# Optimization experiments

Hardware: AMD Instinct MI355X
Metric: run time of the kernel (lower is better)

Reference implementation:

```python
import jax, jax.numpy as jnp
import numpy as np


def reference(x, weight, bias):
    """Per-sample dynamic conv2d, expressed as one grouped convolution.

    x:      (B, C_in, H, W)
    weight: (B, C_out, C_in, kH, kW)
    bias:   (B, C_out)
    returns (B, C_out, H_out, W_out) with H_out = H - kH + 1 (valid conv)
    """
    B, C_in, H, W = x.shape
    C_out, kH, kW = weight.shape[1], weight.shape[3], weight.shape[4]
    # Fold batch into channels: groups=B grouped conv == B independent convs.
    x_g = x.reshape(1, B * C_in, H, W)
    w_g = weight.reshape(B * C_out, C_in, kH, kW)
    out = jax.lax.conv_general_dilated(
        x_g, w_g,
        window_strides=(1, 1),
        padding='VALID',
        dimension_numbers=('NCHW', 'OIHW', 'NCHW'),
        feature_group_count=B,
    )  # (1, B*C_out, H_out, W_out)
    out = out.reshape(B, C_out, out.shape[2], out.shape[3])
    return out + bias[:, :, None, None]


def setup_inputs() -> dict:
    key = jax.random.key(0)
    k1, k2, k3 = jax.random.split(key, 3)
    B, C_in, C_out, H, W, kH, kW = 16, 64, 64, 128, 128, 3, 3
    x = jax.random.normal(k1, (B, C_in, H, W), dtype=jnp.float32)
    weight = jax.random.normal(k2, (B, C_out, C_in, kH, kW), dtype=jnp.float32) * 0.05
    bias = jax.random.normal(k3, (B, C_out), dtype=jnp.float32)
    return {"x": x, "weight": weight, "bias": bias}
```

## Files before the change

kernel.cpp:

```cpp
#include <hip/hip_runtime.h>
#include <hip/hip_bf16.h>

#define BATCH 16
#define CI 64
#define CO 64
#define H 128
#define W 128
#define HO 126
#define WO 126

typedef short bfrag __attribute__((ext_vector_type(8)));
typedef float ffrag __attribute__((ext_vector_type(4)));

static __device__ __forceinline__ unsigned short f2bf(float f) {
    unsigned u = __float_as_uint(f);
    u += 0x7fffu + ((u >> 16) & 1u);
    return (unsigned short)(u >> 16);
}

__global__ void wt_prepass(const float* __restrict__ w, unsigned short* __restrict__ w_t) {
    int i = blockIdx.x * 256 + threadIdx.x;
    int ci = i & 63;
    int co = (i >> 6) & 63;
    int bs = i >> 12;
    int b = bs / 9, s = bs - b * 9;
    w_t[i] = f2bf(w[(((b * 64 + co) * 64 + ci) * 9) + s]);
}

__launch_bounds__(256, 2)
__global__ void dynconv_fused(const float* __restrict__ x,
                              const unsigned short* __restrict__ w_t,
                              const float* __restrict__ bias,
                              float* __restrict__ out) {
    __shared__ __align__(16) unsigned short xs[4 * 8192];

    const int tid  = threadIdx.x;
    const int rg   = blockIdx.x;
    const int b    = blockIdx.y;
    const int y0   = rg * 2;
    const int wave = tid >> 6;
    const int lane = tid & 63;
    const int l16  = lane & 15;
    const int lq   = lane >> 4;
    const int wm   = wave & 1;
    const int wn   = wave >> 1;

    {
        const int col = tid & 127;
        const int h   = tid >> 7;
        const float* xb = x + (size_t)b * CI * H * W + (size_t)y0 * W + col;
        #pragma unroll
        for (int row = 0; row < 4; ++row) {
            #pragma unroll
            for (int oc = 0; oc < 4; ++oc) {
                const int o = h * 4 + oc;
                const float* p = xb + (size_t)(o * 8) * (H * W) + row * W;
                unsigned int u[4];
                #pragma unroll
                for (int e = 0; e < 4; ++e) {
                    float f0 = p[(size_t)(2 * e) * (H * W)];
                    float f1 = p[(size_t)(2 * e + 1) * (H * W)];
                    __hip_bfloat162 h2 = __float22bfloat162_rn(make_float2(f0, f1));
                    u[e] = *(unsigned int*)&h2;
                }
                *(uint4*)&xs[(row * 1024 + col * 8 + (o ^ (col & 7))) * 8] = *(const uint4*)u;
            }
        }
    }

    const bfrag* wtb = (const bfrag*)w_t + (size_t)(b * 9) * 512;
    const int co_b = wm * 32 + l16;
    bfrag acur[4], anxt[4];
    #pragma unroll
    for (int ks = 0; ks < 2; ++ks)
        #pragma unroll
        for (int mt = 0; mt < 2; ++mt)
            acur[ks * 2 + mt] = wtb[(co_b + mt * 16) * 8 + ks * 4 + lq];

    ffrag acc[2][8];
    #pragma unroll
    for (int mt = 0; mt < 2; ++mt)
        #pragma unroll
        for (int nt = 0; nt < 8; ++nt)
            acc[mt][nt] = (ffrag){0.f, 0.f, 0.f, 0.f};

    __syncthreads();

    for (int s = 0; s < 9; ++s) {
        if (s < 8) {
            const bfrag* wn2 = wtb + (s + 1) * 512;
            #pragma unroll
            for (int ks = 0; ks < 2; ++ks)
                #pragma unroll
                for (int mt = 0; mt < 2; ++mt)
                    anxt[ks * 2 + mt] = wn2[(co_b + mt * 16) * 8 + ks * 4 + lq];
        }
        const int dy = s / 3, dx = s - dy * 3;
        const int xr = wn + dy;
        #pragma unroll
        for (int ks = 0; ks < 2; ++ks) {
            const int o = ks * 4 + lq;
            #pragma unroll
            for (int nt = 0; nt < 8; ++nt) {
                int colx = nt * 16 + l16 + dx;
                if (colx > 127) colx = 127;
                const bfrag bf = *(const bfrag*)&xs[xr * 8192 + (colx * 8 + (o ^ (colx & 7))) * 8];
                acc[0][nt] = __builtin_amdgcn_mfma_f32_16x16x32_bf16(acur[ks * 2 + 0], bf, acc[0][nt], 0, 0, 0);
                acc[1][nt] = __builtin_amdgcn_mfma_f32_16x16x32_bf16(acur[ks * 2 + 1], bf, acc[1][nt], 0, 0, 0);
            }
        }
        #pragma unroll
        for (int j = 0; j < 4; ++j) acur[j] = anxt[j];
    }

    const int oy = y0 + wn;
    #pragma unroll
    for (int mt = 0; mt < 2; ++mt) {
        #pragma unroll
        for (int r = 0; r < 4; ++r) {
            int co = wm * 32 + mt * 16 + lq * 4 + r;
            float bv = bias[b * 64 + co];
            float* op = out + ((size_t)(b * 64 + co) * HO + oy) * WO;
            #pragma unroll
            for (int nt = 0; nt < 8; ++nt) {
                int ox = nt * 16 + l16;
                if (ox < WO) op[ox] = acc[mt][nt][r] + bv;
            }
        }
    }
}

extern "C" void kernel_launch(void* const* d_in, const int* in_sizes, int n_in,
                              void* d_out, int out_size, void* d_ws, size_t ws_size,
                              hipStream_t stream) {
    const float* x    = (const float*)d_in[0];
    const float* w    = (const float*)d_in[1];
    const float* bias = (const float*)d_in[2];
    float* out        = (float*)d_out;

    unsigned short* w_t = (unsigned short*)d_ws;

    wt_prepass<<<dim3(589824 / 256), dim3(256), 0, stream>>>(w, w_t);
    dynconv_fused<<<dim3(63, BATCH), dim3(256), 0, stream>>>(x, w_t, bias, out);
}
```

Baseline: 141.3 us.

## Make conv blocks persistent over row pairs with ring-buffered, prefetched input staging

Each block now handles up to four consecutive output row pairs (8 rows) using 512 threads. A 6-slab LDS ring buffer keeps input rows, so each input row is loaded once per block instead of about twice. The next rows are fetched with float4 global loads while the MFMAs for the current pair run, and they are written to LDS after compute. The grid shrinks from 63x16 to 16x16 blocks, which cuts parallelism to 256 blocks. It also adds a barrier per unit and reloads weights from global for every unit.

```diff
diff --git a/kernel.cpp b/kernel.cpp
--- a/kernel.cpp
+++ b/kernel.cpp
@@ -8,6 +8,7 @@
 #define W 128
 #define HO 126
 #define WO 126
+#define HW (H * W)
 
 typedef short bfrag __attribute__((ext_vector_type(8)));
 typedef float ffrag __attribute__((ext_vector_type(4)));
@@ -27,49 +28,63 @@
     w_t[i] = f2bf(w[(((b * 64 + co) * 64 + ci) * 9) + s]);
 }
 
-__launch_bounds__(256, 2)
+__launch_bounds__(512, 2)
 __global__ void dynconv_fused(const float* __restrict__ x,
                               const unsigned short* __restrict__ w_t,
                               const float* __restrict__ bias,
                               float* __restrict__ out) {
-    __shared__ __align__(16) unsigned short xs[4 * 8192];
+    __shared__ __align__(16) unsigned short xs[6 * 8192];
 
-    const int tid  = threadIdx.x;
-    const int rg   = blockIdx.x;
-    const int b    = blockIdx.y;
-    const int y0   = rg * 2;
-    const int wave = tid >> 6;
-    const int lane = tid & 63;
-    const int l16  = lane & 15;
-    const int lq   = lane >> 4;
-    const int wm   = wave & 1;
-    const int wn   = wave >> 1;
+    const int tid = threadIdx.x;
+    const int gx  = blockIdx.x;
+    const int b   = blockIdx.y;
+    const int nunits = (gx == 15) ? 3 : 4;
 
-    {
-        const int col = tid & 127;
-        const int h   = tid >> 7;
-        const float* xb = x + (size_t)b * CI * H * W + (size_t)y0 * W + col;
+    const int wave = tid >> 6, lane = tid & 63;
+    const int l16 = lane & 15, lq = lane >> 4;
+    const int wm = wave & 1;
+    const int wn = (wave >> 1) & 1;
+    const int wc = wave >> 2;
+
+    const int st_r  = tid >> 8;
+    const int st_o  = (tid >> 5) & 7;
+    const int st_cg = tid & 31;
+
+    const float* xb   = x + (size_t)b * CI * HW;
+    const float* stp0 = xb + (size_t)(st_o * 8) * HW + st_cg * 4;
+
+    const int y00 = gx * 8;
+    #pragma unroll
+    for (int pp = 0; pp < 2; ++pp) {
+        const int y = y00 + pp * 2 + st_r;
+        const float* p = stp0 + (size_t)y * W;
+        float4 v[8];
         #pragma unroll
-        for (int row = 0; row < 4; ++row) {
+        for (int e = 0; e < 8; ++e) v[e] = *(const float4*)(p + (size_t)e * HW);
+        const int slab = (y % 6) * 8192;
+        #pragma unroll
+        for (int k = 0; k < 4; ++k) {
+            const int col = st_cg * 4 + k;
+            unsigned int u[4];
             #pragma unroll
-            for (int oc = 0; oc < 4; ++oc) {
-                const int o = h * 4 + oc;
-                const float* p = xb + (size_t)(o * 8) * (H * W) + row * W;
-                unsigned int u[4];
-                #pragma unroll
-                for (int e = 0; e < 4; ++e) {
-                    float f0 = p[(size_t)(2 * e) * (H * W)];
-                    float f1 = p[(size_t)(2 * e + 1) * (H * W)];
-                    __hip_bfloat162 h2 = __float22bfloat162_rn(make_float2(f0, f1));
-                    u[e] = *(unsigned int*)&h2;
-                }
-                *(uint4*)&xs[(row * 1024 + col * 8 + (o ^ (col & 7))) * 8] = *(const uint4*)u;
+            for (int e = 0; e < 4; ++e) {
+                __hip_bfloat162 h2 = __float22bfloat162_rn(
+                    make_float2(((const float*)&v[2 * e])[k], ((const float*)&v[2 * e + 1])[k]));
+                u[e] = *(unsigned int*)&h2;
             }
+            *(uint4*)&xs[slab + (col * 8 + (st_o ^ (col & 7))) * 8] = *(const uint4*)u;
         }
     }
 
     const bfrag* wtb = (const bfrag*)w_t + (size_t)(b * 9) * 512;
     const int co_b = wm * 32 + l16;
+    float bv[2][4];
+    #pragma unroll
+    for (int mt = 0; mt < 2; ++mt)
+        #pragma unroll
+        for (int r = 0; r < 4; ++r)
+            bv[mt][r] = bias[b * 64 + wm * 32 + mt * 16 + lq * 4 + r];
+
     bfrag acur[4], anxt[4];
     #pragma unroll
     for (int ks = 0; ks < 2; ++ks)
@@ -77,54 +92,83 @@
         for (int mt = 0; mt < 2; ++mt)
             acur[ks * 2 + mt] = wtb[(co_b + mt * 16) * 8 + ks * 4 + lq];
 
-    ffrag acc[2][8];
-    #pragma unroll
-    for (int mt = 0; mt < 2; ++mt)
-        #pragma unroll
-        for (int nt = 0; nt < 8; ++nt)
-            acc[mt][nt] = (ffrag){0.f, 0.f, 0.f, 0.f};
-
     __syncthreads();
 
-    for (int s = 0; s < 9; ++s) {
-        if (s < 8) {
-            const bfrag* wn2 = wtb + (s + 1) * 512;
+    for (int j = 0; j < nunits; ++j) {
+        const int y0 = (gx * 4 + j) * 2;
+        const bool hn = (j + 1) < nunits;
+        const int yN = y0 + 4 + st_r;
+
+        float4 v[8];
+        if (hn) {
+            const float* p = stp0 + (size_t)yN * W;
+            #pragma unroll
+            for (int e = 0; e < 8; ++e) v[e] = *(const float4*)(p + (size_t)e * HW);
+        }
+
+        ffrag acc[2][4];
+        #pragma unroll
+        for (int mt = 0; mt < 2; ++mt)
+            #pragma unroll
+            for (int nt = 0; nt < 4; ++nt)
+                acc[mt][nt] = (ffrag){0.f, 0.f, 0.f, 0.f};
+
+        for (int s = 0; s < 9; ++s) {
+            const int sn = (s == 8) ? 0 : s + 1;
+            const bfrag* wnx = wtb + sn * 512;
             #pragma unroll
             for (int ks = 0; ks < 2; ++ks)
                 #pragma unroll
                 for (int mt = 0; mt < 2; ++mt)
-                    anxt[ks * 2 + mt] = wn2[(co_b + mt * 16) * 8 + ks * 4 + lq];
+                    anxt[ks * 2 + mt] = wnx[(co_b + mt * 16) * 8 + ks * 4 + lq];
+
+            const int dy = s / 3, dx = s - dy * 3;
+            const int slab = ((y0 + wn + dy) % 6) * 8192;
+            #pragma unroll
+            for (int ks = 0; ks < 2; ++ks) {
+                const int o = ks * 4 + lq;
+                #pragma unroll
+                for (int nt = 0; nt < 4; ++nt) {
+                    int colx = wc * 64 + nt * 16 + l16 + dx;
+                    if (colx > 127) colx = 127;
+                    const bfrag bf = *(const bfrag*)&xs[slab + (colx * 8 + (o ^ (colx & 7))) * 8];
+                    acc[0][nt] = __builtin_amdgcn_mfma_f32_16x16x32_bf16(acur[ks * 2 + 0], bf, acc[0][nt], 0, 0, 0);
+                    acc[1][nt] = __builtin_amdgcn_mfma_f32_16x16x32_bf16(acur[ks * 2 + 1], bf, acc[1][nt], 0, 0, 0);
+                }
+            }
+            #pragma unroll
+            for (int q = 0; q < 4; ++q) acur[q] = anxt[q];
         }
-        const int dy = s / 3, dx = s - dy * 3;
-        const int xr = wn + dy;
-        #pragma unroll
-        for (int ks = 0; ks < 2; ++ks) {
-            const int o = ks * 4 + lq;
+
+        if (hn) {
+            const int slab = (yN % 6) * 8192;
             #pragma unroll
-            for (int nt = 0; nt < 8; ++nt) {
-                int colx = nt * 16 + l16 + dx;
-                if (colx > 127) colx = 127;
-                const bfrag bf = *(const bfrag*)&xs[xr * 8192 + (colx * 8 + (o ^ (colx & 7))) * 8];
-                acc[0][nt] = __builtin_amdgcn_mfma_f32_16x16x32_bf16(acur[ks * 2 + 0], bf, acc[0][nt], 0, 0, 0);
-                acc[1][nt] = __builtin_amdgcn_mfma_f32_16x16x32_bf16(acur[ks * 2 + 1], bf, acc[1][nt], 0, 0, 0);
+            for (int k = 0; k < 4; ++k) {
+                const int col = st_cg * 4 + k;
+                unsigned int u[4];
+                #pragma unroll
+                for (int e = 0; e < 4; ++e) {
+                    __hip_bfloat162 h2 = __float22bfloat162_rn(
+                        make_float2(((const float*)&v[2 * e])[k], ((const float*)&v[2 * e + 1])[k]));
+                    u[e] = *(unsigned int*)&h2;
+                }
+                *(uint4*)&xs[slab + (col * 8 + (st_o ^ (col & 7))) * 8] = *(const uint4*)u;
             }
         }
+        __syncthreads();
+
+        const int oy = y0 + wn;
         #pragma unroll
-        for (int j = 0; j < 4; ++j) acur[j] = anxt[j];
-    }
-
-    const int oy = y0 + wn;
-    #pragma unroll
-    for (int mt = 0; mt < 2; ++mt) {
-        #pragma unroll
-        for (int r = 0; r < 4; ++r) {
-            int co = wm * 32 + mt * 16 + lq * 4 + r;
-            float bv = bias[b * 64 + co];
-            float* op = out + ((size_t)(b * 64 + co) * HO + oy) * WO;
+        for (int mt = 0; mt < 2; ++mt) {
             #pragma unroll
-            for (int nt = 0; nt < 8; ++nt) {
-                int ox = nt * 16 + l16;
-                if (ox < WO) op[ox] = acc[mt][nt][r] + bv;
+            for (int r = 0; r < 4; ++r) {
+                float* op = out + ((size_t)(b * 64 + wm * 32 + mt * 16 + lq * 4 + r) * HO + oy) * WO;
+                const float bvv = bv[mt][r];
+                #pragma unroll
+                for (int nt = 0; nt < 4; ++nt) {
+                    const int ox = wc * 64 + nt * 16 + l16;
+                    if (ox < WO) op[ox] = acc[mt][nt][r] + bvv;
+                }
             }
         }
     }
@@ -141,5 +185,5 @@
     unsigned short* w_t = (unsigned short*)d_ws;
 
     wt_prepass<<<dim3(589824 / 256), dim3(256), 0, stream>>>(w, w_t);
-    dynconv_fused<<<dim3(63, BATCH), dim3(256), 0, stream>>>(x, w_t, bias, out);
+    dynconv_fused<<<dim3(16, BATCH), dim3(512), 0, stream>>>(x, w_t, bias, out);
 }
```

Result: slower. 173.0 us (+22.5%).
